# Optimization experiments

Measured on AMD Instinct MI355X. Metric: run time of the kernel, lower is better.

## Reference

```python
import jax, jax.numpy as jnp
import numpy as np
import math

B, S, D, H = 2, 4096, 768, 12
HD = D // H  # head_dim = 64


def setup_inputs() -> dict:
    key = jax.random.key(0)
    ks = jax.random.split(key, 12)
    scale = 1.0 / math.sqrt(D)
    inp = {
        "query": jax.random.normal(ks[0], (B, S, D), jnp.float32),
        "key_": jax.random.normal(ks[1], (B, S, D), jnp.float32),
        "value": jax.random.normal(ks[2], (B, S, D), jnp.float32),
        # causal mask: masked_fill where mask == 0
        "mask": jnp.tril(jnp.ones((S, S), jnp.int32))[None, None, :, :],
        "Wq": jax.random.normal(ks[3], (D, D), jnp.float32) * scale,
        "bq": jax.random.normal(ks[4], (D,), jnp.float32) * scale,
        "Wk": jax.random.normal(ks[5], (D, D), jnp.float32) * scale,
        "bk": jax.random.normal(ks[6], (D,), jnp.float32) * scale,
        "Wv": jax.random.normal(ks[7], (D, D), jnp.float32) * scale,
        "bv": jax.random.normal(ks[8], (D,), jnp.float32) * scale,
        "Wo": jax.random.normal(ks[9], (D, D), jnp.float32) * scale,
        "bo": jax.random.normal(ks[10], (D,), jnp.float32) * scale,
    }
    return inp


def reference(query, key_, value, mask, Wq, bq, Wk, bk, Wv, bv, Wo, bo):
    b, s, d = query.shape
    # Linear: x @ W.T + b (torch convention), split heads -> [B, H, S, HD]
    q = (query @ Wq.T + bq).reshape(b, s, H, HD).transpose(0, 2, 1, 3)
    k = (key_ @ Wk.T + bk).reshape(b, s, H, HD).transpose(0, 2, 1, 3)
    v = (value @ Wv.T + bv).reshape(b, s, H, HD).transpose(0, 2, 1, 3)
    # explicit [B, H, S, S] scores as in the source module
    scores = jnp.einsum("bhqd,bhkd->bhqk", q, k) / math.sqrt(HD)
    scores = jnp.where(mask == 0, -jnp.inf, scores)
    attn = jax.nn.softmax(scores, axis=-1)  # dropout p=0.0 -> identity
    out = jnp.einsum("bhqk,bhkd->bhqd", attn, v)
    out = out.transpose(0, 2, 1, 3).reshape(b, s, d)
    return out @ Wo.T + bo
```

## Files before the change

### kernel.cpp

```cpp
#include <hip/hip_runtime.h>

#define Sq 4096
#define Dm 768
#define Hh 12
#define KD 768

typedef short short8 __attribute__((ext_vector_type(8)));
typedef float f32x4 __attribute__((ext_vector_type(4)));
typedef unsigned short bf_t;

__device__ inline bf_t f2bf(float f) {
    unsigned int u = __builtin_bit_cast(unsigned int, f);
    u += 0x7fffu + ((u >> 16) & 1u);
    return (bf_t)(u >> 16);
}

__device__ inline unsigned int pk2bf(float a, float b) {
    unsigned int ua = __builtin_bit_cast(unsigned int, a) + 0x8000u;
    unsigned int ub = __builtin_bit_cast(unsigned int, b) + 0x8000u;
    return __builtin_amdgcn_perm(ub, ua, 0x07060302);
}

__device__ inline float fexp2(float x) {
#if __has_builtin(__builtin_amdgcn_exp2f)
    return __builtin_amdgcn_exp2f(x);
#else
    return exp2f(x);
#endif
}

__device__ inline void gl_lds16(const void* g, void* l) {
    __builtin_amdgcn_global_load_lds(
        (const __attribute__((address_space(1))) unsigned int*)g,
        (__attribute__((address_space(3))) unsigned int*)l, 16, 0, 0);
}

struct CvtJobs { const float* s[4]; bf_t* d[4]; };

__global__ __launch_bounds__(256) void cvt(CvtJobs jobs, int n) {
    const float* s = jobs.s[blockIdx.z];
    bf_t* d = jobs.d[blockIdx.z];
    int i = (blockIdx.x * 256 + threadIdx.x) * 8;
    if (i < n) {
        float4 a = *(const float4*)(s + i);
        float4 b = *(const float4*)(s + i + 4);
        short8 p;
        p[0] = (short)f2bf(a.x); p[1] = (short)f2bf(a.y);
        p[2] = (short)f2bf(a.z); p[3] = (short)f2bf(a.w);
        p[4] = (short)f2bf(b.x); p[5] = (short)f2bf(b.y);
        p[6] = (short)f2bf(b.z); p[7] = (short)f2bf(b.w);
        *(short8*)(d + i) = p;
    }
}

struct GemmJob {
    const bf_t* __restrict__ A; const bf_t* __restrict__ Bm;
    const float* __restrict__ bias; void* __restrict__ out;
    int mode; float scale;
};
struct GemmJobs { GemmJob j[3]; };

__global__ __launch_bounds__(256, 3) void gemm_k(GemmJobs jobs) {
    const GemmJob J = jobs.j[blockIdx.z];
    __shared__ bf_t As[128 * 64];
    __shared__ bf_t Bs[128 * 64];
    const int lane = threadIdx.x & 63, wv = threadIdx.x >> 6;
    const int l16 = lane & 15, quad = lane >> 4;
    const int wm = wv >> 1, wn = wv & 1;
    int m0, n0;
    if (J.mode == 1) { m0 = blockIdx.y * 128; n0 = blockIdx.x * 128; }
    else             { m0 = blockIdx.x * 128; n0 = blockIdx.y * 128; }

    f32x4 acc[4][4] = {};

    for (int kk = 0; kk < KD; kk += 64) {
#pragma unroll
        for (int it = 0; it < 4; ++it) {
            int p0 = it * 256 + wv * 64;
            int p = p0 + lane;
            int row = p >> 3;
            int c = (p & 7) ^ (row & 7);
            gl_lds16(J.A + (size_t)(m0 + row) * KD + kk + c * 8, As + p0 * 8);
            gl_lds16(J.Bm + (size_t)(n0 + row) * KD + kk + c * 8, Bs + p0 * 8);
        }
        __syncthreads();
#pragma unroll
        for (int ks = 0; ks < 2; ++ks) {
            short8 a[4], b[4];
#pragma unroll
            for (int i = 0; i < 4; ++i) {
                int row = wm * 64 + i * 16 + l16;
                int pc = (ks * 4 + quad) ^ (row & 7);
                a[i] = *(const short8*)&As[row * 64 + pc * 8];
            }
#pragma unroll
            for (int j = 0; j < 4; ++j) {
                int row = wn * 64 + j * 16 + l16;
                int pc = (ks * 4 + quad) ^ (row & 7);
                b[j] = *(const short8*)&Bs[row * 64 + pc * 8];
            }
#pragma unroll
            for (int i = 0; i < 4; ++i)
#pragma unroll
                for (int j = 0; j < 4; ++j)
                    acc[i][j] = __builtin_amdgcn_mfma_f32_16x16x32_bf16(a[i], b[j], acc[i][j], 0, 0, 0);
        }
        __syncthreads();
    }

#pragma unroll
    for (int i = 0; i < 4; ++i) {
#pragma unroll
        for (int j = 0; j < 4; ++j) {
            int grow = m0 + wm * 64 + i * 16 + quad * 4;
            int gcol = n0 + wn * 64 + j * 16 + l16;
            if (J.mode == 0) {
                float bv = J.bias[gcol];
                int h = gcol >> 6, hd = gcol & 63;
                bf_t* dst = (bf_t*)J.out;
#pragma unroll
                for (int r = 0; r < 4; ++r) {
                    int row = grow + r;
                    int bI = row >> 12, s = row & 4095;
                    dst[(((size_t)(bI * Hh + h) * Sq + s) << 6) + hd] =
                        f2bf((acc[i][j][r] + bv) * J.scale);
                }
            } else if (J.mode == 1) {
                bf_t* dst = (bf_t*)J.out;
                int t = gcol, bI = t >> 12, s = t & 4095;
                size_t tb = (size_t)(bI * Hh) * Sq * 64;
#pragma unroll
                for (int r = 0; r < 4; ++r) {
                    int f = grow + r;
                    int h = f >> 6, hd = f & 63;
                    dst[tb + (size_t)h * Sq * 64 + (s >> 6) * 4096 + hd * 64 + (s & 63)] =
                        f2bf(acc[i][j][r] + J.bias[f]);
                }
            } else {
                float bv = J.bias[gcol];
                float* dst = (float*)J.out;
#pragma unroll
                for (int r = 0; r < 4; ++r)
                    dst[(size_t)(grow + r) * Dm + gcol] = acc[i][j][r] + bv;
            }
        }
    }
}

#define SHIFT 18.0f
#define NQ 4

__global__ __launch_bounds__(256) void attn(const bf_t* __restrict__ Q,
                                            const bf_t* __restrict__ K,
                                            const bf_t* __restrict__ VT,
                                            bf_t* __restrict__ O) {
    const int bh = blockIdx.x;
    const int qt = gridDim.y - 1 - blockIdx.y;
    const int lane = threadIdx.x & 63, wv = threadIdx.x >> 6;
    const int rg = wv & 1, ksp = wv >> 1;
    const int l16 = lane & 15, quad = lane >> 4;
    const int b = bh / Hh, h = bh % Hh;
    const size_t base = (size_t)bh * Sq * 64;
    const int q0 = qt * 128 + rg * 64;

    __shared__ float ocomb[2][64][68];
    __shared__ float lcomb[2][64];

    const bf_t* __restrict__ Kb = K + base;
    const bf_t* __restrict__ Vb = VT + base;

    short8 qf[NQ][2];
#pragma unroll
    for (int i = 0; i < NQ; ++i) {
        const bf_t* qp = Q + base + (size_t)(q0 + i * 16 + l16) * 64 + quad * 8;
        qf[i][0] = *(const short8*)qp;
        qf[i][1] = *(const short8*)(qp + 32);
    }

    f32x4 oacc[NQ][4] = {};
    f32x4 lsum[NQ] = {};

    const int nkt = (q0 >> 6) + 1;
    const int hsp = (nkt + 1) >> 1;
    const int kt0 = ksp ? hsp : 0;
    const int kt1 = ksp ? nkt : hsp;

    const int kroff = ((l16 >> 2) << 3) + (l16 & 3);

    short8 ones32;
#pragma unroll
    for (int j = 0; j < 8; ++j) ones32[j] = (short)0x3F80;

    short8 kf[4][2];
    short8 vfr[4][2];

    int ko = kroff * 64 + quad * 8 + kt0 * 4096;
    int vo = l16 * 64 + quad * 8 + kt0 * 4096;

#define LOAD_K()                                                             \
    {                                                                        \
        _Pragma("unroll")                                                    \
        for (int g = 0; g < 2; ++g)                                          \
            _Pragma("unroll")                                                \
            for (int s = 0; s < 2; ++s) {                                    \
                const bf_t* kp = Kb + ko + (32 * g + 4 * s) * 64;            \
                kf[2 * g + s][0] = *(const short8*)kp;                       \
                kf[2 * g + s][1] = *(const short8*)(kp + 32);                \
            }                                                                \
    }
#define LOAD_V()                                                             \
    {                                                                        \
        _Pragma("unroll")                                                    \
        for (int ot = 0; ot < 4; ++ot)                                       \
            _Pragma("unroll")                                                \
            for (int g = 0; g < 2; ++g)                                      \
                vfr[ot][g] = *(const short8*)(Vb + vo + ot * 1024 + 32 * g); \
    }

    if (kt0 < kt1) { LOAD_K(); LOAD_V(); }

    for (int kt = kt0; kt < kt1; ++kt) {
        const int kv0 = kt * 64;
        const bool more = (kt + 1 < kt1);
#pragma unroll
        for (int i = 0; i < NQ; ++i) {
            f32x4 st[4];
#pragma unroll
            for (int t = 0; t < 4; ++t) {
                f32x4 z = {-SHIFT, -SHIFT, -SHIFT, -SHIFT};
                z = __builtin_amdgcn_mfma_f32_16x16x32_bf16(kf[t][0], qf[i][0], z, 0, 0, 0);
                st[t] = __builtin_amdgcn_mfma_f32_16x16x32_bf16(kf[t][1], qf[i][1], z, 0, 0, 0);
            }
            if (i == NQ - 1) { ko += 4096; if (more) LOAD_K(); }

            alignas(16) unsigned int pkd[4][2];
            const bool need_mask = (kv0 + 63 > q0 + i * 16);
#pragma unroll
            for (int t = 0; t < 4; ++t) {
                int g = t >> 1, s = t & 1;
                f32x4 sv = st[t];
                if (need_mask) {
                    int qrow = q0 + i * 16 + l16;
                    int kb2 = kv0 + 32 * g + 8 * quad + 4 * s;
#pragma unroll
                    for (int r = 0; r < 4; ++r)
                        if (kb2 + r > qrow) sv[r] = -1e30f;
                }
                pkd[t][0] = pk2bf(fexp2(sv[0]), fexp2(sv[1]));
                pkd[t][1] = pk2bf(fexp2(sv[2]), fexp2(sv[3]));
            }
#pragma unroll
            for (int g = 0; g < 2; ++g) {
                short8 pf = *(const short8*)&pkd[2 * g][0];
                lsum[i] = __builtin_amdgcn_mfma_f32_16x16x32_bf16(ones32, pf, lsum[i], 0, 0, 0);
#pragma unroll
                for (int ot = 0; ot < 4; ++ot)
                    oacc[i][ot] = __builtin_amdgcn_mfma_f32_16x16x32_bf16(vfr[ot][g], pf, oacc[i][ot], 0, 0, 0);
            }
        }
        vo += 4096;
        if (more) LOAD_V();
    }
#undef LOAD_K
#undef LOAD_V

    if (ksp) {
#pragma unroll
        for (int i = 0; i < NQ; ++i) {
            int row = i * 16 + l16;
#pragma unroll
            for (int ot = 0; ot < 4; ++ot)
                *(f32x4*)&ocomb[rg][row][ot * 16 + quad * 4] = oacc[i][ot];
            if (quad == 0) lcomb[rg][row] = lsum[i][0];
        }
    }
    __syncthreads();
    if (!ksp) {
#pragma unroll
        for (int i = 0; i < NQ; ++i) {
            int row = i * 16 + l16;
            float ls = lsum[i][0] + lcomb[rg][row];
            float inv = 1.0f / ls;
            int srow = q0 + row;
            bf_t* orow = O + (size_t)(b * Sq + srow) * Dm + h * 64;
#pragma unroll
            for (int ot = 0; ot < 4; ++ot) {
                f32x4 oc = *(const f32x4*)&ocomb[rg][row][ot * 16 + quad * 4];
                uint2 pk;
                pk.x = pk2bf((oacc[i][ot][0] + oc[0]) * inv, (oacc[i][ot][1] + oc[1]) * inv);
                pk.y = pk2bf((oacc[i][ot][2] + oc[2]) * inv, (oacc[i][ot][3] + oc[3]) * inv);
                *(uint2*)(orow + ot * 16 + quad * 4) = pk;
            }
        }
    }
}

extern "C" void kernel_launch(void* const* d_in, const int* in_sizes, int n_in,
                              void* d_out, int out_size, void* d_ws, size_t ws_size,
                              hipStream_t stream) {
    const float* q  = (const float*)d_in[0];
    const float* k  = (const float*)d_in[1];
    const float* v  = (const float*)d_in[2];
    const float* Wq = (const float*)d_in[4];  const float* bq = (const float*)d_in[5];
    const float* Wk = (const float*)d_in[6];  const float* bk = (const float*)d_in[7];
    const float* Wv = (const float*)d_in[8];  const float* bv = (const float*)d_in[9];
    const float* Wo = (const float*)d_in[10]; const float* bo = (const float*)d_in[11];
    float* out = (float*)d_out;

    const float QSCALE = 0.125f * 1.44269504f;

    const size_t NTOK = (size_t)2 * Sq * Dm;
    const size_t NW   = (size_t)Dm * Dm;
    dim3 b256(256);

    const size_t need_main = (6 * NTOK + 4 * NW) * 2;

    if (ws_size >= need_main) {
        bf_t* qb  = (bf_t*)d_ws;
        bf_t* kb  = qb + NTOK;
        bf_t* vb  = kb + NTOK;
        bf_t* xq  = vb + NTOK;
        bf_t* xk  = xq + NTOK;
        bf_t* xv  = xk + NTOK;
        bf_t* wqb = xv + NTOK;
        bf_t* wkb = wqb + NW;
        bf_t* wvb = wkb + NW;
        bf_t* wob = wvb + NW;
        bf_t* ob  = xq;

        CvtJobs cw = {{Wq, Wk, Wv, Wo}, {wqb, wkb, wvb, wob}};
        cvt<<<dim3(288, 1, 4), b256, 0, stream>>>(cw, (int)NW);
        CvtJobs cx = {{q, k, v, q}, {xq, xk, xv, xq}};
        cvt<<<dim3(3072, 1, 3), b256, 0, stream>>>(cx, (int)NTOK);

        GemmJobs gp;
        gp.j[0] = {xq,  wqb, bq, qb, 0, QSCALE};
        gp.j[1] = {xk,  wkb, bk, kb, 0, 1.0f};
        gp.j[2] = {wvb, xv,  bv, vb, 1, 1.0f};
        gemm_k<<<dim3(64, 6, 3), b256, 0, stream>>>(gp);

        attn<<<dim3(2 * Hh, Sq / 128), b256, 0, stream>>>(qb, kb, vb, ob);

        GemmJobs go;
        go.j[0] = {ob, wob, bo, out, 2, 1.0f};
        go.j[1] = go.j[0]; go.j[2] = go.j[0];
        gemm_k<<<dim3(64, 6, 1), b256, 0, stream>>>(go);
    } else {
        bf_t* qb  = (bf_t*)d_ws;
        bf_t* kb  = qb + NTOK;
        bf_t* vb  = kb + NTOK;
        bf_t* ob  = vb + NTOK;
        bf_t* xc  = ob + NTOK;
        bf_t* wqb = xc + NTOK;
        bf_t* wkb = wqb + NW;
        bf_t* wvb = wkb + NW;
        bf_t* wob = wvb + NW;

        CvtJobs cw = {{Wq, Wk, Wv, Wo}, {wqb, wkb, wvb, wob}};
        cvt<<<dim3(288, 1, 4), b256, 0, stream>>>(cw, (int)NW);

        GemmJobs gj;
        CvtJobs c1 = {{q, q, q, q}, {xc, xc, xc, xc}};
        cvt<<<dim3(3072, 1, 1), b256, 0, stream>>>(c1, (int)NTOK);
        gj.j[0] = {xc, wqb, bq, qb, 0, QSCALE}; gj.j[1] = gj.j[0]; gj.j[2] = gj.j[0];
        gemm_k<<<dim3(64, 6, 1), b256, 0, stream>>>(gj);

        CvtJobs c2 = {{k, k, k, k}, {xc, xc, xc, xc}};
        cvt<<<dim3(3072, 1, 1), b256, 0, stream>>>(c2, (int)NTOK);
        gj.j[0] = {xc, wkb, bk, kb, 0, 1.0f}; gj.j[1] = gj.j[0]; gj.j[2] = gj.j[0];
        gemm_k<<<dim3(64, 6, 1), b256, 0, stream>>>(gj);

        CvtJobs c3 = {{v, v, v, v}, {xc, xc, xc, xc}};
        cvt<<<dim3(3072, 1, 1), b256, 0, stream>>>(c3, (int)NTOK);
        gj.j[0] = {wvb, xc, bv, vb, 1, 1.0f}; gj.j[1] = gj.j[0]; gj.j[2] = gj.j[0];
        gemm_k<<<dim3(64, 6, 1), b256, 0, stream>>>(gj);

        attn<<<dim3(2 * Hh, Sq / 128), b256, 0, stream>>>(qb, kb, vb, ob);

        gj.j[0] = {ob, wob, bo, out, 2, 1.0f}; gj.j[1] = gj.j[0]; gj.j[2] = gj.j[0];
        gemm_k<<<dim3(64, 6, 1), b256, 0, stream>>>(gj);
    }
}
```

Baseline: 362.4 us.

## Share K/V tiles through double-buffered LDS across four query waves

Restructures the attention kernel so each block covers 256 query rows with four waves, each owning 64 rows. K and V tiles are staged cooperatively into swizzled, double-buffered shared memory with direct global-to-LDS loads, replacing per-wave register loads from global memory. This drops the split-KV scheme and its shared-memory combine step. The aim is to cut redundant global K/V traffic by reusing each tile across four waves. In exchange, the grid is halved, a barrier is added every tile, and causal imbalance within a block leaves early waves idle while later ones still work.

```diff
diff --git a/kernel.cpp b/kernel.cpp
--- a/kernel.cpp
+++ b/kernel.cpp
@@ -155,16 +155,17 @@
                                             const bf_t* __restrict__ VT,
                                             bf_t* __restrict__ O) {
     const int bh = blockIdx.x;
-    const int qt = gridDim.y - 1 - blockIdx.y;
-    const int lane = threadIdx.x & 63, wv = threadIdx.x >> 6;
-    const int rg = wv & 1, ksp = wv >> 1;
+    const int y = blockIdx.y;
+    const int lane = threadIdx.x & 63, rg = threadIdx.x >> 6;
     const int l16 = lane & 15, quad = lane >> 4;
     const int b = bh / Hh, h = bh % Hh;
     const size_t base = (size_t)bh * Sq * 64;
-    const int q0 = qt * 128 + rg * 64;
-
-    __shared__ float ocomb[2][64][68];
-    __shared__ float lcomb[2][64];
+    const int q0 = y * 256 + rg * 64;
+    const int nkt_w = (q0 >> 6) + 1;
+    const int kt_max = y * 4 + 4;
+
+    __shared__ bf_t Ks[2][64 * 64];
+    __shared__ bf_t Vs[2][64 * 64];
 
     const bf_t* __restrict__ Kb = K + base;
     const bf_t* __restrict__ Vb = VT + base;
@@ -180,117 +181,104 @@
     f32x4 oacc[NQ][4] = {};
     f32x4 lsum[NQ] = {};
 
-    const int nkt = (q0 >> 6) + 1;
-    const int hsp = (nkt + 1) >> 1;
-    const int kt0 = ksp ? hsp : 0;
-    const int kt1 = ksp ? nkt : hsp;
-
     const int kroff = ((l16 >> 2) << 3) + (l16 & 3);
 
     short8 ones32;
 #pragma unroll
     for (int j = 0; j < 8; ++j) ones32[j] = (short)0x3F80;
 
-    short8 kf[4][2];
-    short8 vfr[4][2];
-
-    int ko = kroff * 64 + quad * 8 + kt0 * 4096;
-    int vo = l16 * 64 + quad * 8 + kt0 * 4096;
-
-#define LOAD_K()                                                             \
+#define STAGE(KT, BUF)                                                       \
     {                                                                        \
+        const bf_t* Ksrc = Kb + (KT) * 4096;                                 \
+        const bf_t* Vsrc = Vb + (KT) * 4096;                                 \
         _Pragma("unroll")                                                    \
-        for (int g = 0; g < 2; ++g)                                          \
-            _Pragma("unroll")                                                \
-            for (int s = 0; s < 2; ++s) {                                    \
-                const bf_t* kp = Kb + ko + (32 * g + 4 * s) * 64;            \
-                kf[2 * g + s][0] = *(const short8*)kp;                       \
-                kf[2 * g + s][1] = *(const short8*)(kp + 32);                \
-            }                                                                \
-    }
-#define LOAD_V()                                                             \
-    {                                                                        \
-        _Pragma("unroll")                                                    \
-        for (int ot = 0; ot < 4; ++ot)                                       \
-            _Pragma("unroll")                                                \
-            for (int g = 0; g < 2; ++g)                                      \
-                vfr[ot][g] = *(const short8*)(Vb + vo + ot * 1024 + 32 * g); \
-    }
-
-    if (kt0 < kt1) { LOAD_K(); LOAD_V(); }
-
-    for (int kt = kt0; kt < kt1; ++kt) {
-        const int kv0 = kt * 64;
-        const bool more = (kt + 1 < kt1);
-#pragma unroll
-        for (int i = 0; i < NQ; ++i) {
-            f32x4 st[4];
-#pragma unroll
-            for (int t = 0; t < 4; ++t) {
-                f32x4 z = {-SHIFT, -SHIFT, -SHIFT, -SHIFT};
-                z = __builtin_amdgcn_mfma_f32_16x16x32_bf16(kf[t][0], qf[i][0], z, 0, 0, 0);
-                st[t] = __builtin_amdgcn_mfma_f32_16x16x32_bf16(kf[t][1], qf[i][1], z, 0, 0, 0);
-            }
-            if (i == NQ - 1) { ko += 4096; if (more) LOAD_K(); }
-
-            alignas(16) unsigned int pkd[4][2];
-            const bool need_mask = (kv0 + 63 > q0 + i * 16);
+        for (int it = 0; it < 2; ++it) {                                     \
+            int p0 = it * 256 + rg * 64;                                     \
+            int p = p0 + lane;                                               \
+            int row = p >> 3;                                                \
+            int c = (p & 7) ^ (row & 7);                                     \
+            gl_lds16(Ksrc + row * 64 + c * 8, &Ks[BUF][p0 * 8]);             \
+            gl_lds16(Vsrc + row * 64 + c * 8, &Vs[BUF][p0 * 8]);             \
+        }                                                                    \
+    }
+
+    STAGE(0, 0);
+    __syncthreads();
+
+    int buf = 0;
+    for (int kt = 0; kt < kt_max; ++kt) {
+        const bool more = (kt + 1 < kt_max);
+        if (more) STAGE(kt + 1, buf ^ 1);
+
+        if (kt < nkt_w) {
+            const int kv0 = kt * 64;
+            short8 kf[4][2];
 #pragma unroll
             for (int t = 0; t < 4; ++t) {
                 int g = t >> 1, s = t & 1;
-                f32x4 sv = st[t];
-                if (need_mask) {
-                    int qrow = q0 + i * 16 + l16;
-                    int kb2 = kv0 + 32 * g + 8 * quad + 4 * s;
-#pragma unroll
-                    for (int r = 0; r < 4; ++r)
-                        if (kb2 + r > qrow) sv[r] = -1e30f;
-                }
-                pkd[t][0] = pk2bf(fexp2(sv[0]), fexp2(sv[1]));
-                pkd[t][1] = pk2bf(fexp2(sv[2]), fexp2(sv[3]));
-            }
-#pragma unroll
-            for (int g = 0; g < 2; ++g) {
-                short8 pf = *(const short8*)&pkd[2 * g][0];
-                lsum[i] = __builtin_amdgcn_mfma_f32_16x16x32_bf16(ones32, pf, lsum[i], 0, 0, 0);
-#pragma unroll
-                for (int ot = 0; ot < 4; ++ot)
-                    oacc[i][ot] = __builtin_amdgcn_mfma_f32_16x16x32_bf16(vfr[ot][g], pf, oacc[i][ot], 0, 0, 0);
-            }
-        }
-        vo += 4096;
-        if (more) LOAD_V();
-    }
-#undef LOAD_K
-#undef LOAD_V
-
-    if (ksp) {
-#pragma unroll
-        for (int i = 0; i < NQ; ++i) {
-            int row = i * 16 + l16;
-#pragma unroll
-            for (int ot = 0; ot < 4; ++ot)
-                *(f32x4*)&ocomb[rg][row][ot * 16 + quad * 4] = oacc[i][ot];
-            if (quad == 0) lcomb[rg][row] = lsum[i][0];
-        }
-    }
-    __syncthreads();
-    if (!ksp) {
-#pragma unroll
-        for (int i = 0; i < NQ; ++i) {
-            int row = i * 16 + l16;
-            float ls = lsum[i][0] + lcomb[rg][row];
-            float inv = 1.0f / ls;
-            int srow = q0 + row;
-            bf_t* orow = O + (size_t)(b * Sq + srow) * Dm + h * 64;
+                int row = 32 * g + 4 * s + kroff;
+                kf[t][0] = *(const short8*)&Ks[buf][row * 64 + ((quad) ^ (row & 7)) * 8];
+                kf[t][1] = *(const short8*)&Ks[buf][row * 64 + ((4 + quad) ^ (row & 7)) * 8];
+            }
+            short8 vfr[4][2];
 #pragma unroll
             for (int ot = 0; ot < 4; ++ot) {
-                f32x4 oc = *(const f32x4*)&ocomb[rg][row][ot * 16 + quad * 4];
-                uint2 pk;
-                pk.x = pk2bf((oacc[i][ot][0] + oc[0]) * inv, (oacc[i][ot][1] + oc[1]) * inv);
-                pk.y = pk2bf((oacc[i][ot][2] + oc[2]) * inv, (oacc[i][ot][3] + oc[3]) * inv);
-                *(uint2*)(orow + ot * 16 + quad * 4) = pk;
-            }
+                int row = ot * 16 + l16;
+#pragma unroll
+                for (int g = 0; g < 2; ++g)
+                    vfr[ot][g] = *(const short8*)&Vs[buf][row * 64 + ((4 * g + quad) ^ (row & 7)) * 8];
+            }
+#pragma unroll
+            for (int i = 0; i < NQ; ++i) {
+                f32x4 st[4];
+#pragma unroll
+                for (int t = 0; t < 4; ++t) {
+                    f32x4 z = {-SHIFT, -SHIFT, -SHIFT, -SHIFT};
+                    z = __builtin_amdgcn_mfma_f32_16x16x32_bf16(kf[t][0], qf[i][0], z, 0, 0, 0);
+                    st[t] = __builtin_amdgcn_mfma_f32_16x16x32_bf16(kf[t][1], qf[i][1], z, 0, 0, 0);
+                }
+                alignas(16) unsigned int pkd[4][2];
+                const bool need_mask = (kv0 + 63 > q0 + i * 16);
+#pragma unroll
+                for (int t = 0; t < 4; ++t) {
+                    int g = t >> 1, s = t & 1;
+                    f32x4 sv = st[t];
+                    if (need_mask) {
+                        int qrow = q0 + i * 16 + l16;
+                        int kb2 = kv0 + 32 * g + 8 * quad + 4 * s;
+#pragma unroll
+                        for (int r = 0; r < 4; ++r)
+                            if (kb2 + r > qrow) sv[r] = -1e30f;
+                    }
+                    pkd[t][0] = pk2bf(fexp2(sv[0]), fexp2(sv[1]));
+                    pkd[t][1] = pk2bf(fexp2(sv[2]), fexp2(sv[3]));
+                }
+#pragma unroll
+                for (int g = 0; g < 2; ++g) {
+                    short8 pf = *(const short8*)&pkd[2 * g][0];
+                    lsum[i] = __builtin_amdgcn_mfma_f32_16x16x32_bf16(ones32, pf, lsum[i], 0, 0, 0);
+#pragma unroll
+                    for (int ot = 0; ot < 4; ++ot)
+                        oacc[i][ot] = __builtin_amdgcn_mfma_f32_16x16x32_bf16(vfr[ot][g], pf, oacc[i][ot], 0, 0, 0);
+                }
+            }
+        }
+        __syncthreads();
+        buf ^= 1;
+    }
+#undef STAGE
+
+#pragma unroll
+    for (int i = 0; i < NQ; ++i) {
+        float inv = 1.0f / lsum[i][0];
+        int srow = q0 + i * 16 + l16;
+        bf_t* orow = O + (size_t)(b * Sq + srow) * Dm + h * 64;
+#pragma unroll
+        for (int ot = 0; ot < 4; ++ot) {
+            uint2 pk;
+            pk.x = pk2bf(oacc[i][ot][0] * inv, oacc[i][ot][1] * inv);
+            pk.y = pk2bf(oacc[i][ot][2] * inv, oacc[i][ot][3] * inv);
+            *(uint2*)(orow + ot * 16 + quad * 4) = pk;
         }
     }
 }
@@ -339,7 +327,7 @@
         gp.j[2] = {wvb, xv,  bv, vb, 1, 1.0f};
         gemm_k<<<dim3(64, 6, 3), b256, 0, stream>>>(gp);
 
-        attn<<<dim3(2 * Hh, Sq / 128), b256, 0, stream>>>(qb, kb, vb, ob);
+        attn<<<dim3(2 * Hh, Sq / 256), b256, 0, stream>>>(qb, kb, vb, ob);
 
         GemmJobs go;
         go.j[0] = {ob, wob, bo, out, 2, 1.0f};
@@ -375,7 +363,7 @@
         gj.j[0] = {wvb, xc, bv, vb, 1, 1.0f}; gj.j[1] = gj.j[0]; gj.j[2] = gj.j[0];
         gemm_k<<<dim3(64, 6, 1), b256, 0, stream>>>(gj);
 
-        attn<<<dim3(2 * Hh, Sq / 128), b256, 0, stream>>>(qb, kb, vb, ob);
+        attn<<<dim3(2 * Hh, Sq / 256), b256, 0, stream>>>(qb, kb, vb, ob);
 
         gj.j[0] = {ob, wob, bo, out, 2, 1.0f}; gj.j[1] = gj.j[0]; gj.j[2] = gj.j[0];
         gemm_k<<<dim3(64, 6, 1), b256, 0, stream>>>(gj);
```

New measurement: 423.4 us. 1.17x slower.
